# Optimization experiments

Measured on AMD Instinct MI355X. Metric: run time of the kernel, lower is better.

## Reference

```python
import jax, jax.numpy as jnp
import numpy as np

EPS = 1e-8
LAM = 100.0
SINKHORN_ITER = 50


def _sinkhorn(pred, target, cost, lam, n_iter):
    # pred: (B, na), target: (B, nb), cost: (na, nb)
    na = pred.shape[1]
    nb = target.shape[1]
    cost = cost[:na, :nb]
    K = jnp.exp(-cost / lam)          # (na, nb)
    KM = cost * K                      # (na, nb)
    B = pred.shape[0]
    log_a = jnp.log(pred + EPS)
    log_b = jnp.log(target + EPS)
    log_u0 = jnp.full((B, na), -np.log(na), dtype=pred.dtype)
    log_v0 = jnp.full((B, nb), -np.log(nb), dtype=pred.dtype)

    def cond(state):
        i, _, _, done = state
        return (i < n_iter) & jnp.logical_not(done)

    def body(state):
        i, log_u, log_v, done = state
        log_u_max = jnp.max(log_u, axis=1, keepdims=True)
        # NOTE: original code adds EPS inside the exp here (kept for fidelity)
        u_stab = jnp.exp(log_u - log_u_max + EPS)
        # torch.mm(K.t(), u_stab.t()).t() == u_stab @ K
        log_v_new = log_b - jnp.log(u_stab @ K) - log_u_max
        log_v_max = jnp.max(log_v_new, axis=1, keepdims=True)
        v_stab = jnp.exp(log_v_new - log_v_max)
        log_u_new = log_a - jnp.log(v_stab @ K.T + EPS) - log_v_max
        # early-exit convergence check (relative Frobenius norm)
        done_new = (jnp.linalg.norm(log_u - log_u_new) /
                    jnp.linalg.norm(log_u_new)) < EPS
        return (i + 1, log_u_new, log_v_new, done_new)

    _, log_u, log_v, _ = jax.lax.while_loop(
        cond, body, (jnp.int32(0), log_u0, log_v0, jnp.array(False)))

    log_v_max = jnp.max(log_v, axis=1, keepdims=True)
    v_stab = jnp.exp(log_v - log_v_max)
    logcostpart1 = jnp.log(v_stab @ KM.T + EPS) + log_v_max
    wnorm = jnp.exp(log_u + logcostpart1).mean(0).sum()
    grad_input = log_u * lam
    grad_input = grad_input - grad_input.mean(axis=1, keepdims=True)
    grad_input = grad_input - grad_input.mean(axis=1, keepdims=True)
    grad_input = grad_input / B
    return wnorm.reshape(1), grad_input


def setup_inputs() -> dict:
    key = jax.random.key(0)
    k1, k2, k3 = jax.random.split(key, 3)
    B, na, nb = 65536, 128, 128
    pred = jax.random.uniform(k1, (B, na), dtype=jnp.float32)
    target = jax.random.uniform(k2, (B, nb), dtype=jnp.float32)
    cost = jax.random.uniform(k3, (na, nb), dtype=jnp.float32)
    return {"pred": pred, "target": target, "cost": cost}


def reference(pred, target, cost):
    return _sinkhorn(pred, target, cost, LAM, SINKHORN_ITER)
```

## Files before the change

kernel.cpp:

```cpp
#include <hip/hip_runtime.h>
#include <hip/hip_bf16.h>


typedef __attribute__((ext_vector_type(4))) float f32x4;
typedef __attribute__((ext_vector_type(4))) short s16x4;
typedef __attribute__((ext_vector_type(8))) short s16x8;

constexpr int   BLOCK = 512;
constexpr float EPSF  = 1e-8f;
constexpr float LOG2E = 1.44269504088896340736f;
constexpr float LN2   = 0.69314718055994530942f;
constexpr float GRADS = LN2 * 100.0f / 65536.0f;


#define SGB_PAIR() do {                                      \
    __builtin_amdgcn_sched_group_barrier(0x100, 2, 0);       \
    __builtin_amdgcn_sched_group_barrier(0x008, 1, 0);       \
  } while (0)

__device__ __forceinline__ unsigned short f2bf(float x) {
  unsigned u = __builtin_bit_cast(unsigned, x);
  u += 0x7fffu + ((u >> 16) & 1u);
  return (unsigned short)(u >> 16);
}
__device__ __forceinline__ float bf2f(short h) {
  return __builtin_bit_cast(float, (unsigned)(unsigned short)h << 16);
}
__device__ __forceinline__ short f2bf_hot(float x) {
  return __builtin_bit_cast(short, __float2bfloat16(x));
}

__device__ __forceinline__ int swzw(int r, int c) {
  return (r << 7) + ((((c >> 2) ^ ((r & 7) << 2)) << 2) | (c & 3));
}

__device__ __forceinline__ s16x8 afrag(const short* M, int row, int kb, int h) {
  const int base = (row << 7) + ((((kb >> 2) + h) ^ ((row & 7) << 2)) << 2);
  const s16x4 lo = *reinterpret_cast<const s16x4*>(M + base);
  const s16x4 hi = *reinterpret_cast<const s16x4*>(M + (base ^ 16));
  s16x8 r;
  r[0] = lo[0]; r[1] = lo[1]; r[2] = lo[2]; r[3] = lo[3];
  r[4] = hi[0]; r[5] = hi[1]; r[6] = hi[2]; r[7] = hi[3];
  return r;
}

__device__ __forceinline__ s16x8 packb(const f32x4 a, const f32x4 b) {
  s16x8 r;
  r[0] = f2bf_hot(a[0]); r[1] = f2bf_hot(a[1]);
  r[2] = f2bf_hot(a[2]); r[3] = f2bf_hot(a[3]);
  r[4] = f2bf_hot(b[0]); r[5] = f2bf_hot(b[1]);
  r[6] = f2bf_hot(b[2]); r[7] = f2bf_hot(b[3]);
  return r;
}

__global__ __launch_bounds__(256)
void sink_pre(const float* __restrict__ cost, unsigned short* __restrict__ wh,
              float* __restrict__ Sf)
{
  const float c1 = LOG2E * 0.01f;
  const int tid = threadIdx.x;
  if (blockIdx.x < 32) {
    for (int idx = blockIdx.x * 256 + tid; idx < 16384; idx += 8192) {
      const int r = idx >> 7, c = idx & 127;
      const float cst = cost[idx];
      const float k   = __builtin_amdgcn_exp2f(-cst * c1);
      const unsigned short eb = f2bf(k - 1.0f);
      wh[swzw(r, c)]          = eb;
      wh[16384 + swzw(c, r)]  = eb;
      wh[32768 + swzw(r, c)]  = f2bf(cst * k);
    }
  } else {
    __shared__ float ps[256];
    const int i = tid & 127, jh = tid >> 7;
    float s = 0.f;
#pragma unroll 8
    for (int j = jh * 64; j < jh * 64 + 64; ++j)
      s += __builtin_amdgcn_exp2f(-cost[(j << 7) + i] * c1);
    ps[tid] = s;
    __syncthreads();
    if (tid < 128) Sf[tid] = ps[tid] + ps[tid + 128];
  }
}

__global__ __launch_bounds__(BLOCK, 4)
void sink_mfma(const float* __restrict__ pred,
               const float* __restrict__ tgt,
               const unsigned short* __restrict__ wh,
               const float* __restrict__ Sf,
               float* __restrict__ out,
               float* __restrict__ wsf)
{
  __shared__ __align__(16) short EA[128 * 128];
  __shared__ __align__(16) short EB[128 * 128];
  __shared__ float wred[8];

  const int tid  = threadIdx.x;
  const int lane = tid & 63;
  const int wv   = tid >> 6;
  const int cl   = lane & 15;
  const int h    = lane >> 4;

  const int row0 = (blockIdx.x << 7) + (wv << 4);
  const int rr   = (row0 + cl) << 7;

  float4 p4[8], t4[8], s4[8];
#pragma unroll
  for (int mt = 0; mt < 8; ++mt) {
    p4[mt] = *reinterpret_cast<const float4*>(&pred[rr + (mt << 4) + (h << 2)]);
    t4[mt] = *reinterpret_cast<const float4*>(&tgt [rr + (mt << 4) + (h << 2)]);
    s4[mt] = *reinterpret_cast<const float4*>(&Sf[(mt << 4) + (h << 2)]);
  }

  {
    const uint4* gB = reinterpret_cast<const uint4*>(wh);
    const uint4* gA = reinterpret_cast<const uint4*>(wh + 16384);
    uint4* lB = reinterpret_cast<uint4*>(EB);
    uint4* lA = reinterpret_cast<uint4*>(EA);
#pragma unroll
    for (int k = 0; k < 4; ++k) {
      lB[tid + k * BLOCK] = gB[tid + k * BLOCK];
      lA[tid + k * BLOCK] = gA[tid + k * BLOCK];
    }
  }

  s16x8 ab[4], bb[4], vf[4], uf[4];
  f32x4 X[8];
  float sum_v = 0.f;
#pragma unroll
  for (int mt = 0; mt < 8; ++mt) {
    f32x4 qa, qb, v;
    qa[0] = p4[mt].x + EPSF; qa[1] = p4[mt].y + EPSF;
    qa[2] = p4[mt].z + EPSF; qa[3] = p4[mt].w + EPSF;
    qb[0] = t4[mt].x + EPSF; qb[1] = t4[mt].y + EPSF;
    qb[2] = t4[mt].z + EPSF; qb[3] = t4[mt].w + EPSF;
    v[0] = qb[0] * __builtin_amdgcn_rcpf(s4[mt].x);
    v[1] = qb[1] * __builtin_amdgcn_rcpf(s4[mt].y);
    v[2] = qb[2] * __builtin_amdgcn_rcpf(s4[mt].z);
    v[3] = qb[3] * __builtin_amdgcn_rcpf(s4[mt].w);
    sum_v += v[0] + v[1] + v[2] + v[3];
    X[mt] = v;
#pragma unroll
    for (int q = 0; q < 4; ++q) {
      ab[mt >> 1][(mt & 1) * 4 + q] = f2bf_hot(qa[q]);
      bb[mt >> 1][(mt & 1) * 4 + q] = f2bf_hot(qb[q]);
    }
  }
#pragma unroll
  for (int s = 0; s < 4; ++s) vf[s] = packb(X[2 * s], X[2 * s + 1]);
  sum_v += __shfl_xor(sum_v, 16);
  sum_v += __shfl_xor(sum_v, 32);
  __syncthreads();

#pragma unroll
  for (int mt = 0; mt < 8; ++mt) X[mt] = f32x4{0, 0, 0, 0};
#pragma unroll
  for (int s = 0; s < 4; ++s)
#pragma unroll
    for (int mt = 0; mt < 8; ++mt) {
      X[mt] = __builtin_amdgcn_mfma_f32_16x16x32_bf16(
          afrag(EB, cl + (mt << 4), s << 5, h), vf[s], X[mt], 0, 0, 0);
      SGB_PAIR();
    }
  float sum_u = 0.f;
#pragma unroll
  for (int mt = 0; mt < 8; ++mt)
#pragma unroll
    for (int q = 0; q < 4; ++q) {
      const float a = bf2f(ab[mt >> 1][(mt & 1) * 4 + q]);
      const float r = a * __builtin_amdgcn_rcpf(sum_v + X[mt][q] + EPSF);
      X[mt][q] = r;
      sum_u += r;
    }
#pragma unroll
  for (int s = 0; s < 4; ++s) uf[s] = packb(X[2 * s], X[2 * s + 1]);
  sum_u += __shfl_xor(sum_u, 16);
  sum_u += __shfl_xor(sum_u, 32);

#pragma unroll
  for (int mt = 0; mt < 8; ++mt) X[mt] = f32x4{0, 0, 0, 0};
#pragma unroll
  for (int s = 0; s < 4; ++s)
#pragma unroll
    for (int mt = 0; mt < 8; ++mt) {
      X[mt] = __builtin_amdgcn_mfma_f32_16x16x32_bf16(
          afrag(EA, cl + (mt << 4), s << 5, h), uf[s], X[mt], 0, 0, 0);
      SGB_PAIR();
    }
  sum_v = 0.f;
#pragma unroll
  for (int mt = 0; mt < 8; ++mt)
#pragma unroll
    for (int q = 0; q < 4; ++q) {
      const float b = bf2f(bb[mt >> 1][(mt & 1) * 4 + q]);
      const float v = b * __builtin_amdgcn_rcpf(sum_u + X[mt][q]);
      X[mt][q] = v;
      sum_v += v;
    }
#pragma unroll
  for (int s = 0; s < 4; ++s) vf[s] = packb(X[2 * s], X[2 * s + 1]);
  sum_v += __shfl_xor(sum_v, 16);
  sum_v += __shfl_xor(sum_v, 32);

#pragma unroll
  for (int mt = 0; mt < 8; ++mt) X[mt] = f32x4{0, 0, 0, 0};
#pragma unroll
  for (int s = 0; s < 4; ++s)
#pragma unroll
    for (int mt = 0; mt < 8; ++mt) {
      X[mt] = __builtin_amdgcn_mfma_f32_16x16x32_bf16(
          afrag(EB, cl + (mt << 4), s << 5, h), vf[s], X[mt], 0, 0, 0);
      SGB_PAIR();
    }
#pragma unroll
  for (int mt = 0; mt < 8; ++mt)
#pragma unroll
    for (int q = 0; q < 4; ++q) {
      const float a = bf2f(ab[mt >> 1][(mt & 1) * 4 + q]);
      X[mt][q] = a * __builtin_amdgcn_rcpf(sum_v + X[mt][q] + EPSF);
    }

  __syncthreads();
  {
    const uint4* gK = reinterpret_cast<const uint4*>(wh + 32768);
    uint4* lB = reinterpret_cast<uint4*>(EB);
#pragma unroll
    for (int k = 0; k < 4; ++k) lB[tid + k * BLOCK] = gK[tid + k * BLOCK];
  }
  __syncthreads();

  f32x4 T[8];
#pragma unroll
  for (int mt = 0; mt < 8; ++mt) T[mt] = f32x4{0, 0, 0, 0};
#pragma unroll
  for (int s = 0; s < 4; ++s)
#pragma unroll
    for (int mt = 0; mt < 8; ++mt) {
      T[mt] = __builtin_amdgcn_mfma_f32_16x16x32_bf16(
          afrag(EB, cl + (mt << 4), s << 5, h), vf[s], T[mt], 0, 0, 0);
      SGB_PAIR();
    }

  float wsum = 0.f;
#pragma unroll
  for (int mt = 0; mt < 8; ++mt)
#pragma unroll
    for (int q = 0; q < 4; ++q)
      wsum += X[mt][q] * (T[mt][q] + EPSF);
  wsum += __shfl_xor(wsum, 1);
  wsum += __shfl_xor(wsum, 2);
  wsum += __shfl_xor(wsum, 4);
  wsum += __shfl_xor(wsum, 8);
  wsum += __shfl_xor(wsum, 16);
  wsum += __shfl_xor(wsum, 32);
  if (lane == 0) wred[wv] = wsum;

  {
#pragma unroll
    for (int mt = 0; mt < 8; ++mt)
#pragma unroll
      for (int q = 0; q < 4; ++q)
        X[mt][q] = __builtin_amdgcn_logf(X[mt][q]);
    float sm = 0.f;
#pragma unroll
    for (int mt = 0; mt < 8; ++mt)
#pragma unroll
      for (int q = 0; q < 4; ++q) sm += X[mt][q];
    sm += __shfl_xor(sm, 16);
    sm += __shfl_xor(sm, 32);
    const float mean = sm * 0.0078125f;

    float* TAf = reinterpret_cast<float*>(EA);
    const int obase = 1 + (blockIdx.x << 14);
    const int lrow  = (wv & 3) << 4;
#pragma unroll
    for (int half = 0; half < 2; ++half) {
      __syncthreads();
      if ((wv >> 2) == half) {
#pragma unroll
        for (int mt = 0; mt < 8; ++mt)
#pragma unroll
          for (int q = 0; q < 4; ++q) {
            const int col = (mt << 4) + (h << 2) + q;
            TAf[((lrow + cl) << 7) + (col ^ ((cl & 7) << 2))] =
                (X[mt][q] - mean) * GRADS;
          }
      }
      __syncthreads();
#pragma unroll
      for (int k = 0; k < 16; ++k) {
        const int lin = k * BLOCK + tid;
        const int row = lin >> 7, col = lin & 127;
        out[obase + (half << 13) + lin] =
            TAf[(row << 7) + (col ^ ((row & 7) << 2))];
      }
    }
  }

  __syncthreads();
  if (tid == 0) {
    float s = 0.f;
#pragma unroll
    for (int w = 0; w < 8; ++w) s += wred[w];
    wsf[blockIdx.x] = s;
  }
}

__global__ void sink_reduce(const float* __restrict__ wsf, float* __restrict__ out)
{
  float s = 0.f;
  for (int i = threadIdx.x; i < 512; i += 256) s += wsf[i];
  s += __shfl_xor(s, 1);
  s += __shfl_xor(s, 2);
  s += __shfl_xor(s, 4);
  s += __shfl_xor(s, 8);
  s += __shfl_xor(s, 16);
  s += __shfl_xor(s, 32);
  __shared__ float sm[4];
  if ((threadIdx.x & 63) == 0) sm[threadIdx.x >> 6] = s;
  __syncthreads();
  if (threadIdx.x == 0) out[0] = (sm[0] + sm[1] + sm[2] + sm[3]) * (1.0f / 65536.0f);
}

extern "C" void kernel_launch(void* const* d_in, const int* in_sizes, int n_in,
                              void* d_out, int out_size, void* d_ws, size_t ws_size,
                              hipStream_t stream)
{
  const float* pred = (const float*)d_in[0];
  const float* tgt  = (const float*)d_in[1];
  const float* cost = (const float*)d_in[2];
  float* out = (float*)d_out;
  unsigned short* wh = (unsigned short*)d_ws;
  float* Sf  = ((float*)d_ws) + 24576;
  float* wsf = ((float*)d_ws) + 24704;

  sink_pre<<<33, 256, 0, stream>>>(cost, wh, Sf);
  sink_mfma<<<512, BLOCK, 0, stream>>>(pred, tgt, wh, Sf, out, wsf);
  sink_reduce<<<1, 256, 0, stream>>>(wsf, out);
}
```

Measured before the change: 44.77 us.

## Process two row tiles per block with all tables resident in LDS

Each block now handles 256 rows in two sequential tiles instead of 128 rows. All three bf16 tables (E, E^T, K*M) are loaded into LDS once, so the block no longer reloads the cost table mid-kernel behind extra barriers. The next tile's pred and target are prefetched during the current tile. The final E and KM matmuls are fused into one interleaved MFMA loop, and the output transpose goes through a per-wave LDS buffer without block-wide barriers. In exchange the grid halves to 256 blocks, shared memory per block grows, and the launch-bounds occupancy hint drops to 2, which may cut latency hiding.

```diff
diff --git a/kernel.cpp b/kernel.cpp
--- a/kernel.cpp
+++ b/kernel.cpp
@@ -16,6 +16,10 @@
 #define SGB_PAIR() do {                                      \
     __builtin_amdgcn_sched_group_barrier(0x100, 2, 0);       \
     __builtin_amdgcn_sched_group_barrier(0x008, 1, 0);       \
+  } while (0)
+#define SGB_QUAD() do {                                      \
+    __builtin_amdgcn_sched_group_barrier(0x100, 4, 0);       \
+    __builtin_amdgcn_sched_group_barrier(0x008, 2, 0);       \
   } while (0)
 
 __device__ __forceinline__ unsigned short f2bf(float x) {
@@ -82,7 +86,7 @@
   }
 }
 
-__global__ __launch_bounds__(BLOCK, 4)
+__global__ __launch_bounds__(BLOCK, 2)
 void sink_mfma(const float* __restrict__ pred,
                const float* __restrict__ tgt,
                const unsigned short* __restrict__ wh,
@@ -90,9 +94,12 @@
                float* __restrict__ out,
                float* __restrict__ wsf)
 {
-  __shared__ __align__(16) short EA[128 * 128];
-  __shared__ __align__(16) short EB[128 * 128];
-  __shared__ float wred[8];
+  __shared__ __align__(16) short TBL[3 * 16384];
+  __shared__ __align__(16) float TR[8 * 1024];
+
+  const short* Es  = TBL;
+  const short* ETs = TBL + 16384;
+  const short* KMs = TBL + 32768;
 
   const int tid  = threadIdx.x;
   const int lane = tid & 63;
@@ -100,207 +107,196 @@
   const int cl   = lane & 15;
   const int h    = lane >> 4;
 
-  const int row0 = (blockIdx.x << 7) + (wv << 4);
-  const int rr   = (row0 + cl) << 7;
-
-  float4 p4[8], t4[8], s4[8];
+  const int rr0 = (((blockIdx.x << 8) + (wv << 4) + cl) << 7) + (h << 2);
+  float4 p4[8], t4[8], rs[8];
 #pragma unroll
   for (int mt = 0; mt < 8; ++mt) {
-    p4[mt] = *reinterpret_cast<const float4*>(&pred[rr + (mt << 4) + (h << 2)]);
-    t4[mt] = *reinterpret_cast<const float4*>(&tgt [rr + (mt << 4) + (h << 2)]);
-    s4[mt] = *reinterpret_cast<const float4*>(&Sf[(mt << 4) + (h << 2)]);
+    p4[mt] = *reinterpret_cast<const float4*>(&pred[rr0 + (mt << 4)]);
+    t4[mt] = *reinterpret_cast<const float4*>(&tgt [rr0 + (mt << 4)]);
+    const float4 s = *reinterpret_cast<const float4*>(&Sf[(mt << 4) + (h << 2)]);
+    rs[mt].x = __builtin_amdgcn_rcpf(s.x);
+    rs[mt].y = __builtin_amdgcn_rcpf(s.y);
+    rs[mt].z = __builtin_amdgcn_rcpf(s.z);
+    rs[mt].w = __builtin_amdgcn_rcpf(s.w);
   }
 
   {
-    const uint4* gB = reinterpret_cast<const uint4*>(wh);
-    const uint4* gA = reinterpret_cast<const uint4*>(wh + 16384);
-    uint4* lB = reinterpret_cast<uint4*>(EB);
-    uint4* lA = reinterpret_cast<uint4*>(EA);
-#pragma unroll
-    for (int k = 0; k < 4; ++k) {
-      lB[tid + k * BLOCK] = gB[tid + k * BLOCK];
-      lA[tid + k * BLOCK] = gA[tid + k * BLOCK];
-    }
-  }
-
-  s16x8 ab[4], bb[4], vf[4], uf[4];
-  f32x4 X[8];
-  float sum_v = 0.f;
-#pragma unroll
-  for (int mt = 0; mt < 8; ++mt) {
-    f32x4 qa, qb, v;
-    qa[0] = p4[mt].x + EPSF; qa[1] = p4[mt].y + EPSF;
-    qa[2] = p4[mt].z + EPSF; qa[3] = p4[mt].w + EPSF;
-    qb[0] = t4[mt].x + EPSF; qb[1] = t4[mt].y + EPSF;
-    qb[2] = t4[mt].z + EPSF; qb[3] = t4[mt].w + EPSF;
-    v[0] = qb[0] * __builtin_amdgcn_rcpf(s4[mt].x);
-    v[1] = qb[1] * __builtin_amdgcn_rcpf(s4[mt].y);
-    v[2] = qb[2] * __builtin_amdgcn_rcpf(s4[mt].z);
-    v[3] = qb[3] * __builtin_amdgcn_rcpf(s4[mt].w);
-    sum_v += v[0] + v[1] + v[2] + v[3];
-    X[mt] = v;
-#pragma unroll
-    for (int q = 0; q < 4; ++q) {
-      ab[mt >> 1][(mt & 1) * 4 + q] = f2bf_hot(qa[q]);
-      bb[mt >> 1][(mt & 1) * 4 + q] = f2bf_hot(qb[q]);
-    }
-  }
-#pragma unroll
-  for (int s = 0; s < 4; ++s) vf[s] = packb(X[2 * s], X[2 * s + 1]);
-  sum_v += __shfl_xor(sum_v, 16);
-  sum_v += __shfl_xor(sum_v, 32);
+    const uint4* g = reinterpret_cast<const uint4*>(wh);
+    uint4* l = reinterpret_cast<uint4*>(TBL);
+#pragma unroll
+    for (int k = 0; k < 12; ++k) l[tid + k * BLOCK] = g[tid + k * BLOCK];
+  }
   __syncthreads();
 
-#pragma unroll
-  for (int mt = 0; mt < 8; ++mt) X[mt] = f32x4{0, 0, 0, 0};
-#pragma unroll
-  for (int s = 0; s < 4; ++s)
+  float wacc = 0.f;
+  float* TRw = TR + (wv << 10);
+
+#pragma unroll
+  for (int tile = 0; tile < 2; ++tile) {
+    s16x8 ab[4], bb[4], vf[4], uf[4];
+    f32x4 X[8], T[8];
+    float sum_v = 0.f;
 #pragma unroll
     for (int mt = 0; mt < 8; ++mt) {
-      X[mt] = __builtin_amdgcn_mfma_f32_16x16x32_bf16(
-          afrag(EB, cl + (mt << 4), s << 5, h), vf[s], X[mt], 0, 0, 0);
-      SGB_PAIR();
-    }
-  float sum_u = 0.f;
-#pragma unroll
-  for (int mt = 0; mt < 8; ++mt)
-#pragma unroll
-    for (int q = 0; q < 4; ++q) {
-      const float a = bf2f(ab[mt >> 1][(mt & 1) * 4 + q]);
-      const float r = a * __builtin_amdgcn_rcpf(sum_v + X[mt][q] + EPSF);
-      X[mt][q] = r;
-      sum_u += r;
-    }
-#pragma unroll
-  for (int s = 0; s < 4; ++s) uf[s] = packb(X[2 * s], X[2 * s + 1]);
-  sum_u += __shfl_xor(sum_u, 16);
-  sum_u += __shfl_xor(sum_u, 32);
-
-#pragma unroll
-  for (int mt = 0; mt < 8; ++mt) X[mt] = f32x4{0, 0, 0, 0};
-#pragma unroll
-  for (int s = 0; s < 4; ++s)
+      f32x4 qa, qb, v;
+      qa[0] = p4[mt].x + EPSF; qa[1] = p4[mt].y + EPSF;
+      qa[2] = p4[mt].z + EPSF; qa[3] = p4[mt].w + EPSF;
+      qb[0] = t4[mt].x + EPSF; qb[1] = t4[mt].y + EPSF;
+      qb[2] = t4[mt].z + EPSF; qb[3] = t4[mt].w + EPSF;
+      v[0] = qb[0] * rs[mt].x; v[1] = qb[1] * rs[mt].y;
+      v[2] = qb[2] * rs[mt].z; v[3] = qb[3] * rs[mt].w;
+      sum_v += v[0] + v[1] + v[2] + v[3];
+      X[mt] = v;
+#pragma unroll
+      for (int q = 0; q < 4; ++q) {
+        ab[mt >> 1][(mt & 1) * 4 + q] = f2bf_hot(qa[q]);
+        bb[mt >> 1][(mt & 1) * 4 + q] = f2bf_hot(qb[q]);
+      }
+    }
+#pragma unroll
+    for (int s = 0; s < 4; ++s) vf[s] = packb(X[2 * s], X[2 * s + 1]);
+    sum_v += __shfl_xor(sum_v, 16);
+    sum_v += __shfl_xor(sum_v, 32);
+
+    if (tile == 0) {
+      const int rr1 = rr0 + (128 << 7);
+#pragma unroll
+      for (int mt = 0; mt < 8; ++mt) {
+        p4[mt] = *reinterpret_cast<const float4*>(&pred[rr1 + (mt << 4)]);
+        t4[mt] = *reinterpret_cast<const float4*>(&tgt [rr1 + (mt << 4)]);
+      }
+    }
+
+#pragma unroll
+    for (int mt = 0; mt < 8; ++mt) X[mt] = f32x4{0, 0, 0, 0};
+#pragma unroll
+    for (int s = 0; s < 4; ++s)
+#pragma unroll
+      for (int mt = 0; mt < 8; ++mt) {
+        X[mt] = __builtin_amdgcn_mfma_f32_16x16x32_bf16(
+            afrag(Es, cl + (mt << 4), s << 5, h), vf[s], X[mt], 0, 0, 0);
+        SGB_PAIR();
+      }
+    float sum_u = 0.f;
+#pragma unroll
+    for (int mt = 0; mt < 8; ++mt)
+#pragma unroll
+      for (int q = 0; q < 4; ++q) {
+        const float a = bf2f(ab[mt >> 1][(mt & 1) * 4 + q]);
+        const float r = a * __builtin_amdgcn_rcpf(sum_v + X[mt][q] + EPSF);
+        X[mt][q] = r;
+        sum_u += r;
+      }
+#pragma unroll
+    for (int s = 0; s < 4; ++s) uf[s] = packb(X[2 * s], X[2 * s + 1]);
+    sum_u += __shfl_xor(sum_u, 16);
+    sum_u += __shfl_xor(sum_u, 32);
+
+#pragma unroll
+    for (int mt = 0; mt < 8; ++mt) X[mt] = f32x4{0, 0, 0, 0};
+#pragma unroll
+    for (int s = 0; s < 4; ++s)
+#pragma unroll
+      for (int mt = 0; mt < 8; ++mt) {
+        X[mt] = __builtin_amdgcn_mfma_f32_16x16x32_bf16(
+            afrag(ETs, cl + (mt << 4), s << 5, h), uf[s], X[mt], 0, 0, 0);
+        SGB_PAIR();
+      }
+    sum_v = 0.f;
+#pragma unroll
+    for (int mt = 0; mt < 8; ++mt)
+#pragma unroll
+      for (int q = 0; q < 4; ++q) {
+        const float b = bf2f(bb[mt >> 1][(mt & 1) * 4 + q]);
+        const float v = b * __builtin_amdgcn_rcpf(sum_u + X[mt][q]);
+        X[mt][q] = v;
+        sum_v += v;
+      }
+#pragma unroll
+    for (int s = 0; s < 4; ++s) vf[s] = packb(X[2 * s], X[2 * s + 1]);
+    sum_v += __shfl_xor(sum_v, 16);
+    sum_v += __shfl_xor(sum_v, 32);
+
 #pragma unroll
     for (int mt = 0; mt < 8; ++mt) {
-      X[mt] = __builtin_amdgcn_mfma_f32_16x16x32_bf16(
-          afrag(EA, cl + (mt << 4), s << 5, h), uf[s], X[mt], 0, 0, 0);
-      SGB_PAIR();
-    }
-  sum_v = 0.f;
-#pragma unroll
-  for (int mt = 0; mt < 8; ++mt)
-#pragma unroll
-    for (int q = 0; q < 4; ++q) {
-      const float b = bf2f(bb[mt >> 1][(mt & 1) * 4 + q]);
-      const float v = b * __builtin_amdgcn_rcpf(sum_u + X[mt][q]);
-      X[mt][q] = v;
-      sum_v += v;
-    }
-#pragma unroll
-  for (int s = 0; s < 4; ++s) vf[s] = packb(X[2 * s], X[2 * s + 1]);
-  sum_v += __shfl_xor(sum_v, 16);
-  sum_v += __shfl_xor(sum_v, 32);
-
-#pragma unroll
-  for (int mt = 0; mt < 8; ++mt) X[mt] = f32x4{0, 0, 0, 0};
-#pragma unroll
-  for (int s = 0; s < 4; ++s)
-#pragma unroll
-    for (int mt = 0; mt < 8; ++mt) {
-      X[mt] = __builtin_amdgcn_mfma_f32_16x16x32_bf16(
-          afrag(EB, cl + (mt << 4), s << 5, h), vf[s], X[mt], 0, 0, 0);
-      SGB_PAIR();
-    }
-#pragma unroll
-  for (int mt = 0; mt < 8; ++mt)
-#pragma unroll
-    for (int q = 0; q < 4; ++q) {
-      const float a = bf2f(ab[mt >> 1][(mt & 1) * 4 + q]);
-      X[mt][q] = a * __builtin_amdgcn_rcpf(sum_v + X[mt][q] + EPSF);
-    }
-
+      X[mt] = f32x4{0, 0, 0, 0};
+      T[mt] = f32x4{0, 0, 0, 0};
+    }
+#pragma unroll
+    for (int s = 0; s < 4; ++s)
+#pragma unroll
+      for (int mt = 0; mt < 8; ++mt) {
+        X[mt] = __builtin_amdgcn_mfma_f32_16x16x32_bf16(
+            afrag(Es, cl + (mt << 4), s << 5, h), vf[s], X[mt], 0, 0, 0);
+        T[mt] = __builtin_amdgcn_mfma_f32_16x16x32_bf16(
+            afrag(KMs, cl + (mt << 4), s << 5, h), vf[s], T[mt], 0, 0, 0);
+        SGB_QUAD();
+      }
+#pragma unroll
+    for (int mt = 0; mt < 8; ++mt)
+#pragma unroll
+      for (int q = 0; q < 4; ++q) {
+        const float a = bf2f(ab[mt >> 1][(mt & 1) * 4 + q]);
+        X[mt][q] = a * __builtin_amdgcn_rcpf(sum_v + X[mt][q] + EPSF);
+      }
+
+#pragma unroll
+    for (int mt = 0; mt < 8; ++mt)
+#pragma unroll
+      for (int q = 0; q < 4; ++q)
+        wacc += X[mt][q] * (T[mt][q] + EPSF);
+
+    {
+#pragma unroll
+      for (int mt = 0; mt < 8; ++mt)
+#pragma unroll
+        for (int q = 0; q < 4; ++q)
+          X[mt][q] = __builtin_amdgcn_logf(X[mt][q]);
+      float sm = 0.f;
+#pragma unroll
+      for (int mt = 0; mt < 8; ++mt)
+#pragma unroll
+        for (int q = 0; q < 4; ++q) sm += X[mt][q];
+      sm += __shfl_xor(sm, 16);
+      sm += __shfl_xor(sm, 32);
+      const float mean = sm * 0.0078125f;
+
+      const int owave = 1 + ((((blockIdx.x << 1) + tile) << 7) + (wv << 4)) * 128;
+      const int rloc = cl & 7;
+#pragma unroll
+      for (int p = 0; p < 2; ++p) {
+        if ((cl >> 3) == p) {
+#pragma unroll
+          for (int mt = 0; mt < 8; ++mt)
+#pragma unroll
+            for (int q = 0; q < 4; ++q) {
+              const int col = (mt << 4) + (h << 2) + q;
+              TRw[(rloc << 7) + (col ^ (rloc << 2))] = (X[mt][q] - mean) * GRADS;
+            }
+        }
+#pragma unroll
+        for (int k = 0; k < 16; ++k) {
+          const int lin = k * 64 + lane;
+          const int r = lin >> 7, c = lin & 127;
+          out[owave + (p << 10) + lin] = TRw[(r << 7) + (c ^ (r << 2))];
+        }
+      }
+    }
+  }
+
+  wacc += __shfl_xor(wacc, 1);
+  wacc += __shfl_xor(wacc, 2);
+  wacc += __shfl_xor(wacc, 4);
+  wacc += __shfl_xor(wacc, 8);
+  wacc += __shfl_xor(wacc, 16);
+  wacc += __shfl_xor(wacc, 32);
   __syncthreads();
-  {
-    const uint4* gK = reinterpret_cast<const uint4*>(wh + 32768);
-    uint4* lB = reinterpret_cast<uint4*>(EB);
-#pragma unroll
-    for (int k = 0; k < 4; ++k) lB[tid + k * BLOCK] = gK[tid + k * BLOCK];
-  }
-  __syncthreads();
-
-  f32x4 T[8];
-#pragma unroll
-  for (int mt = 0; mt < 8; ++mt) T[mt] = f32x4{0, 0, 0, 0};
-#pragma unroll
-  for (int s = 0; s < 4; ++s)
-#pragma unroll
-    for (int mt = 0; mt < 8; ++mt) {
-      T[mt] = __builtin_amdgcn_mfma_f32_16x16x32_bf16(
-          afrag(EB, cl + (mt << 4), s << 5, h), vf[s], T[mt], 0, 0, 0);
-      SGB_PAIR();
-    }
-
-  float wsum = 0.f;
-#pragma unroll
-  for (int mt = 0; mt < 8; ++mt)
-#pragma unroll
-    for (int q = 0; q < 4; ++q)
-      wsum += X[mt][q] * (T[mt][q] + EPSF);
-  wsum += __shfl_xor(wsum, 1);
-  wsum += __shfl_xor(wsum, 2);
-  wsum += __shfl_xor(wsum, 4);
-  wsum += __shfl_xor(wsum, 8);
-  wsum += __shfl_xor(wsum, 16);
-  wsum += __shfl_xor(wsum, 32);
-  if (lane == 0) wred[wv] = wsum;
-
-  {
-#pragma unroll
-    for (int mt = 0; mt < 8; ++mt)
-#pragma unroll
-      for (int q = 0; q < 4; ++q)
-        X[mt][q] = __builtin_amdgcn_logf(X[mt][q]);
-    float sm = 0.f;
-#pragma unroll
-    for (int mt = 0; mt < 8; ++mt)
-#pragma unroll
-      for (int q = 0; q < 4; ++q) sm += X[mt][q];
-    sm += __shfl_xor(sm, 16);
-    sm += __shfl_xor(sm, 32);
-    const float mean = sm * 0.0078125f;
-
-    float* TAf = reinterpret_cast<float*>(EA);
-    const int obase = 1 + (blockIdx.x << 14);
-    const int lrow  = (wv & 3) << 4;
-#pragma unroll
-    for (int half = 0; half < 2; ++half) {
-      __syncthreads();
-      if ((wv >> 2) == half) {
-#pragma unroll
-        for (int mt = 0; mt < 8; ++mt)
-#pragma unroll
-          for (int q = 0; q < 4; ++q) {
-            const int col = (mt << 4) + (h << 2) + q;
-            TAf[((lrow + cl) << 7) + (col ^ ((cl & 7) << 2))] =
-                (X[mt][q] - mean) * GRADS;
-          }
-      }
-      __syncthreads();
-#pragma unroll
-      for (int k = 0; k < 16; ++k) {
-        const int lin = k * BLOCK + tid;
-        const int row = lin >> 7, col = lin & 127;
-        out[obase + (half << 13) + lin] =
-            TAf[(row << 7) + (col ^ ((row & 7) << 2))];
-      }
-    }
-  }
-
+  if (lane == 0) TR[wv] = wacc;
   __syncthreads();
   if (tid == 0) {
     float s = 0.f;
 #pragma unroll
-    for (int w = 0; w < 8; ++w) s += wred[w];
+    for (int w = 0; w < 8; ++w) s += TR[w];
     wsf[blockIdx.x] = s;
   }
 }
@@ -308,7 +304,7 @@
 __global__ void sink_reduce(const float* __restrict__ wsf, float* __restrict__ out)
 {
   float s = 0.f;
-  for (int i = threadIdx.x; i < 512; i += 256) s += wsf[i];
+  for (int i = threadIdx.x; i < 256; i += 256) s += wsf[i];
   s += __shfl_xor(s, 1);
   s += __shfl_xor(s, 2);
   s += __shfl_xor(s, 4);
@@ -334,6 +330,6 @@
   float* wsf = ((float*)d_ws) + 24704;
 
   sink_pre<<<33, 256, 0, stream>>>(cost, wh, Sf);
-  sink_mfma<<<512, BLOCK, 0, stream>>>(pred, tgt, wh, Sf, out, wsf);
+  sink_mfma<<<256, BLOCK, 0, stream>>>(pred, tgt, wh, Sf, out, wsf);
   sink_reduce<<<1, 256, 0, stream>>>(wsf, out);
 }
```

After: 59.02 us. 31.8% more time.

## Fuse final reduction into main kernel via last-block atomic; prefetch KM weights

Applied to the files above, without the earlier changes.

Removes the separate sink_reduce launch by having each block publish its partial sum with a release store and bump an atomic counter, so the last block finishes the reduction. The KM weight matrix is now read from global memory into registers at kernel start and written into the freed EA buffer before the final Sinkhorn matvec, which removes one global-load stall and one barrier. MFMA/LDS-read scheduling barriers are regrouped from pairs into groups of eight. The cost is extra register pressure from holding KM in registers, plus a counter reset in the pre-kernel.

```diff
diff --git a/kernel.cpp b/kernel.cpp
--- a/kernel.cpp
+++ b/kernel.cpp
@@ -13,9 +13,9 @@
 constexpr float GRADS = LN2 * 100.0f / 65536.0f;
 
 
-#define SGB_PAIR() do {                                      \
-    __builtin_amdgcn_sched_group_barrier(0x100, 2, 0);       \
-    __builtin_amdgcn_sched_group_barrier(0x008, 1, 0);       \
+#define SGB_G8() do {                                        \
+    __builtin_amdgcn_sched_group_barrier(0x100, 8, 0);       \
+    __builtin_amdgcn_sched_group_barrier(0x008, 4, 0);       \
   } while (0)
 
 __device__ __forceinline__ unsigned short f2bf(float x) {
@@ -55,7 +55,7 @@
 
 __global__ __launch_bounds__(256)
 void sink_pre(const float* __restrict__ cost, unsigned short* __restrict__ wh,
-              float* __restrict__ Sf)
+              float* __restrict__ Sf, unsigned* __restrict__ cnt)
 {
   const float c1 = LOG2E * 0.01f;
   const int tid = threadIdx.x;
@@ -70,6 +70,7 @@
       wh[32768 + swzw(r, c)]  = f2bf(cst * k);
     }
   } else {
+    if (tid == 0) *cnt = 0u;
     __shared__ float ps[256];
     const int i = tid & 127, jh = tid >> 7;
     float s = 0.f;
@@ -88,11 +89,13 @@
                const unsigned short* __restrict__ wh,
                const float* __restrict__ Sf,
                float* __restrict__ out,
-               float* __restrict__ wsf)
+               float* __restrict__ wsf,
+               unsigned* __restrict__ cnt)
 {
   __shared__ __align__(16) short EA[128 * 128];
   __shared__ __align__(16) short EB[128 * 128];
   __shared__ float wred[8];
+  __shared__ unsigned lastflag;
 
   const int tid  = threadIdx.x;
   const int lane = tid & 63;
@@ -104,11 +107,17 @@
   const int rr   = (row0 + cl) << 7;
 
   float4 p4[8], t4[8], s4[8];
+  uint4 kmr[4];
 #pragma unroll
   for (int mt = 0; mt < 8; ++mt) {
     p4[mt] = *reinterpret_cast<const float4*>(&pred[rr + (mt << 4) + (h << 2)]);
     t4[mt] = *reinterpret_cast<const float4*>(&tgt [rr + (mt << 4) + (h << 2)]);
     s4[mt] = *reinterpret_cast<const float4*>(&Sf[(mt << 4) + (h << 2)]);
+  }
+  {
+    const uint4* gK = reinterpret_cast<const uint4*>(wh + 32768);
+#pragma unroll
+    for (int k = 0; k < 4; ++k) kmr[k] = gK[tid + k * BLOCK];
   }
 
   {
@@ -159,7 +168,7 @@
     for (int mt = 0; mt < 8; ++mt) {
       X[mt] = __builtin_amdgcn_mfma_f32_16x16x32_bf16(
           afrag(EB, cl + (mt << 4), s << 5, h), vf[s], X[mt], 0, 0, 0);
-      SGB_PAIR();
+      if ((mt & 3) == 3) SGB_G8();
     }
   float sum_u = 0.f;
 #pragma unroll
@@ -184,7 +193,7 @@
     for (int mt = 0; mt < 8; ++mt) {
       X[mt] = __builtin_amdgcn_mfma_f32_16x16x32_bf16(
           afrag(EA, cl + (mt << 4), s << 5, h), uf[s], X[mt], 0, 0, 0);
-      SGB_PAIR();
+      if ((mt & 3) == 3) SGB_G8();
     }
   sum_v = 0.f;
 #pragma unroll
@@ -201,6 +210,13 @@
   sum_v += __shfl_xor(sum_v, 16);
   sum_v += __shfl_xor(sum_v, 32);
 
+  __syncthreads();
+  {
+    uint4* lA = reinterpret_cast<uint4*>(EA);
+#pragma unroll
+    for (int k = 0; k < 4; ++k) lA[tid + k * BLOCK] = kmr[k];
+  }
+
 #pragma unroll
   for (int mt = 0; mt < 8; ++mt) X[mt] = f32x4{0, 0, 0, 0};
 #pragma unroll
@@ -209,7 +225,7 @@
     for (int mt = 0; mt < 8; ++mt) {
       X[mt] = __builtin_amdgcn_mfma_f32_16x16x32_bf16(
           afrag(EB, cl + (mt << 4), s << 5, h), vf[s], X[mt], 0, 0, 0);
-      SGB_PAIR();
+      if ((mt & 3) == 3) SGB_G8();
     }
 #pragma unroll
   for (int mt = 0; mt < 8; ++mt)
@@ -218,14 +234,6 @@
       const float a = bf2f(ab[mt >> 1][(mt & 1) * 4 + q]);
       X[mt][q] = a * __builtin_amdgcn_rcpf(sum_v + X[mt][q] + EPSF);
     }
-
-  __syncthreads();
-  {
-    const uint4* gK = reinterpret_cast<const uint4*>(wh + 32768);
-    uint4* lB = reinterpret_cast<uint4*>(EB);
-#pragma unroll
-    for (int k = 0; k < 4; ++k) lB[tid + k * BLOCK] = gK[tid + k * BLOCK];
-  }
   __syncthreads();
 
   f32x4 T[8];
@@ -236,8 +244,8 @@
 #pragma unroll
     for (int mt = 0; mt < 8; ++mt) {
       T[mt] = __builtin_amdgcn_mfma_f32_16x16x32_bf16(
-          afrag(EB, cl + (mt << 4), s << 5, h), vf[s], T[mt], 0, 0, 0);
-      SGB_PAIR();
+          afrag(EA, cl + (mt << 4), s << 5, h), vf[s], T[mt], 0, 0, 0);
+      if ((mt & 3) == 3) SGB_G8();
     }
 
   float wsum = 0.f;
@@ -301,24 +309,26 @@
     float s = 0.f;
 #pragma unroll
     for (int w = 0; w < 8; ++w) s += wred[w];
-    wsf[blockIdx.x] = s;
-  }
-}
-
-__global__ void sink_reduce(const float* __restrict__ wsf, float* __restrict__ out)
-{
-  float s = 0.f;
-  for (int i = threadIdx.x; i < 512; i += 256) s += wsf[i];
-  s += __shfl_xor(s, 1);
-  s += __shfl_xor(s, 2);
-  s += __shfl_xor(s, 4);
-  s += __shfl_xor(s, 8);
-  s += __shfl_xor(s, 16);
-  s += __shfl_xor(s, 32);
-  __shared__ float sm[4];
-  if ((threadIdx.x & 63) == 0) sm[threadIdx.x >> 6] = s;
-  __syncthreads();
-  if (threadIdx.x == 0) out[0] = (sm[0] + sm[1] + sm[2] + sm[3]) * (1.0f / 65536.0f);
+    __hip_atomic_store(&wsf[blockIdx.x], s, __ATOMIC_RELEASE,
+                       __HIP_MEMORY_SCOPE_AGENT);
+    const unsigned prev = __hip_atomic_fetch_add(cnt, 1u, __ATOMIC_ACQ_REL,
+                                                 __HIP_MEMORY_SCOPE_AGENT);
+    lastflag = (prev == 511u) ? 1u : 0u;
+  }
+  __syncthreads();
+  if (lastflag != 0u && wv == 0) {
+    float s = 0.f;
+    for (int i = lane; i < 512; i += 64)
+      s += __hip_atomic_load(&wsf[i], __ATOMIC_ACQUIRE,
+                             __HIP_MEMORY_SCOPE_AGENT);
+    s += __shfl_xor(s, 1);
+    s += __shfl_xor(s, 2);
+    s += __shfl_xor(s, 4);
+    s += __shfl_xor(s, 8);
+    s += __shfl_xor(s, 16);
+    s += __shfl_xor(s, 32);
+    if (lane == 0) out[0] = s * (1.0f / 65536.0f);
+  }
 }
 
 extern "C" void kernel_launch(void* const* d_in, const int* in_sizes, int n_in,
@@ -332,8 +342,8 @@
   unsigned short* wh = (unsigned short*)d_ws;
   float* Sf  = ((float*)d_ws) + 24576;
   float* wsf = ((float*)d_ws) + 24704;
-
-  sink_pre<<<33, 256, 0, stream>>>(cost, wh, Sf);
-  sink_mfma<<<512, BLOCK, 0, stream>>>(pred, tgt, wh, Sf, out, wsf);
-  sink_reduce<<<1, 256, 0, stream>>>(wsf, out);
-}
+  unsigned* cnt = (unsigned*)(((float*)d_ws) + 25216);
+
+  sink_pre<<<33, 256, 0, stream>>>(cost, wh, Sf, cnt);
+  sink_mfma<<<512, BLOCK, 0, stream>>>(pred, tgt, wh, Sf, out, wsf, cnt);
+}
```

Result: slower. 101.8 us (+127.5%).

## Process two 16-row tiles per wave to reuse LDS A-fragments across MFMAs

Applied to the files above, without the earlier changes.

Halves the block to 256 threads, with each wave now handling 32 rows as two 16-row N-tiles. Each A-fragment read from LDS feeds two MFMAs, halving LDS traffic per MFMA, and the schedule barrier is adjusted to pair 2 MFMAs with 2 LDS reads. Reciprocals of the column sums are hoisted and shared. The cost is doubled accumulator and fragment register use with launch bounds dropped to 2 blocks per CU, which lowers occupancy and the latency hiding it provides.

```diff
diff --git a/kernel.cpp b/kernel.cpp
--- a/kernel.cpp
+++ b/kernel.cpp
@@ -6,16 +6,16 @@
 typedef __attribute__((ext_vector_type(4))) short s16x4;
 typedef __attribute__((ext_vector_type(8))) short s16x8;
 
-constexpr int   BLOCK = 512;
+constexpr int   BLOCK = 256;
 constexpr float EPSF  = 1e-8f;
 constexpr float LOG2E = 1.44269504088896340736f;
 constexpr float LN2   = 0.69314718055994530942f;
 constexpr float GRADS = LN2 * 100.0f / 65536.0f;
 
 
-#define SGB_PAIR() do {                                      \
+#define SGB_22() do {                                        \
     __builtin_amdgcn_sched_group_barrier(0x100, 2, 0);       \
-    __builtin_amdgcn_sched_group_barrier(0x008, 1, 0);       \
+    __builtin_amdgcn_sched_group_barrier(0x008, 2, 0);       \
   } while (0)
 
 __device__ __forceinline__ unsigned short f2bf(float x) {
@@ -82,7 +82,7 @@
   }
 }
 
-__global__ __launch_bounds__(BLOCK, 4)
+__global__ __launch_bounds__(BLOCK, 2)
 void sink_mfma(const float* __restrict__ pred,
                const float* __restrict__ tgt,
                const unsigned short* __restrict__ wh,
@@ -92,7 +92,7 @@
 {
   __shared__ __align__(16) short EA[128 * 128];
   __shared__ __align__(16) short EB[128 * 128];
-  __shared__ float wred[8];
+  __shared__ float wred[4];
 
   const int tid  = threadIdx.x;
   const int lane = tid & 63;
@@ -100,15 +100,24 @@
   const int cl   = lane & 15;
   const int h    = lane >> 4;
 
-  const int row0 = (blockIdx.x << 7) + (wv << 4);
-  const int rr   = (row0 + cl) << 7;
-
-  float4 p4[8], t4[8], s4[8];
+  const int row0 = (blockIdx.x << 7) + (wv << 5);
+
+  float4 rs[8], p4[8], t4[8];
 #pragma unroll
   for (int mt = 0; mt < 8; ++mt) {
-    p4[mt] = *reinterpret_cast<const float4*>(&pred[rr + (mt << 4) + (h << 2)]);
-    t4[mt] = *reinterpret_cast<const float4*>(&tgt [rr + (mt << 4) + (h << 2)]);
-    s4[mt] = *reinterpret_cast<const float4*>(&Sf[(mt << 4) + (h << 2)]);
+    const float4 s = *reinterpret_cast<const float4*>(&Sf[(mt << 4) + (h << 2)]);
+    rs[mt].x = __builtin_amdgcn_rcpf(s.x);
+    rs[mt].y = __builtin_amdgcn_rcpf(s.y);
+    rs[mt].z = __builtin_amdgcn_rcpf(s.z);
+    rs[mt].w = __builtin_amdgcn_rcpf(s.w);
+  }
+  {
+    const int rr = ((row0 + cl) << 7) + (h << 2);
+#pragma unroll
+    for (int mt = 0; mt < 8; ++mt) {
+      p4[mt] = *reinterpret_cast<const float4*>(&pred[rr + (mt << 4)]);
+      t4[mt] = *reinterpret_cast<const float4*>(&tgt [rr + (mt << 4)]);
+    }
   }
 
   {
@@ -117,177 +126,212 @@
     uint4* lB = reinterpret_cast<uint4*>(EB);
     uint4* lA = reinterpret_cast<uint4*>(EA);
 #pragma unroll
-    for (int k = 0; k < 4; ++k) {
+    for (int k = 0; k < 8; ++k) {
       lB[tid + k * BLOCK] = gB[tid + k * BLOCK];
       lA[tid + k * BLOCK] = gA[tid + k * BLOCK];
     }
   }
 
-  s16x8 ab[4], bb[4], vf[4], uf[4];
-  f32x4 X[8];
-  float sum_v = 0.f;
-#pragma unroll
-  for (int mt = 0; mt < 8; ++mt) {
-    f32x4 qa, qb, v;
-    qa[0] = p4[mt].x + EPSF; qa[1] = p4[mt].y + EPSF;
-    qa[2] = p4[mt].z + EPSF; qa[3] = p4[mt].w + EPSF;
-    qb[0] = t4[mt].x + EPSF; qb[1] = t4[mt].y + EPSF;
-    qb[2] = t4[mt].z + EPSF; qb[3] = t4[mt].w + EPSF;
-    v[0] = qb[0] * __builtin_amdgcn_rcpf(s4[mt].x);
-    v[1] = qb[1] * __builtin_amdgcn_rcpf(s4[mt].y);
-    v[2] = qb[2] * __builtin_amdgcn_rcpf(s4[mt].z);
-    v[3] = qb[3] * __builtin_amdgcn_rcpf(s4[mt].w);
-    sum_v += v[0] + v[1] + v[2] + v[3];
-    X[mt] = v;
-#pragma unroll
-    for (int q = 0; q < 4; ++q) {
-      ab[mt >> 1][(mt & 1) * 4 + q] = f2bf_hot(qa[q]);
-      bb[mt >> 1][(mt & 1) * 4 + q] = f2bf_hot(qb[q]);
-    }
-  }
-#pragma unroll
-  for (int s = 0; s < 4; ++s) vf[s] = packb(X[2 * s], X[2 * s + 1]);
-  sum_v += __shfl_xor(sum_v, 16);
-  sum_v += __shfl_xor(sum_v, 32);
-  __syncthreads();
-
-#pragma unroll
-  for (int mt = 0; mt < 8; ++mt) X[mt] = f32x4{0, 0, 0, 0};
+  s16x8 ab[2][4], bb[2][4], vf[2][4], uf[2][4];
+  f32x4 X[2][8];
+  float sum_v[2], sum_u[2];
+#pragma unroll
+  for (int nt = 0; nt < 2; ++nt) {
+    if (nt == 1) {
+      const int rr = ((row0 + 16 + cl) << 7) + (h << 2);
+#pragma unroll
+      for (int mt = 0; mt < 8; ++mt) {
+        p4[mt] = *reinterpret_cast<const float4*>(&pred[rr + (mt << 4)]);
+        t4[mt] = *reinterpret_cast<const float4*>(&tgt [rr + (mt << 4)]);
+      }
+    }
+    float sv = 0.f;
+#pragma unroll
+    for (int mt = 0; mt < 8; ++mt) {
+      f32x4 qa, qb, v;
+      qa[0] = p4[mt].x + EPSF; qa[1] = p4[mt].y + EPSF;
+      qa[2] = p4[mt].z + EPSF; qa[3] = p4[mt].w + EPSF;
+      qb[0] = t4[mt].x + EPSF; qb[1] = t4[mt].y + EPSF;
+      qb[2] = t4[mt].z + EPSF; qb[3] = t4[mt].w + EPSF;
+      v[0] = qb[0] * rs[mt].x; v[1] = qb[1] * rs[mt].y;
+      v[2] = qb[2] * rs[mt].z; v[3] = qb[3] * rs[mt].w;
+      sv += v[0] + v[1] + v[2] + v[3];
+      X[nt][mt] = v;
+#pragma unroll
+      for (int q = 0; q < 4; ++q) {
+        ab[nt][mt >> 1][(mt & 1) * 4 + q] = f2bf_hot(qa[q]);
+        bb[nt][mt >> 1][(mt & 1) * 4 + q] = f2bf_hot(qb[q]);
+      }
+    }
+#pragma unroll
+    for (int s = 0; s < 4; ++s) vf[nt][s] = packb(X[nt][2 * s], X[nt][2 * s + 1]);
+    sv += __shfl_xor(sv, 16);
+    sv += __shfl_xor(sv, 32);
+    sum_v[nt] = sv;
+  }
+  __syncthreads();
+
+#pragma unroll
+  for (int mt = 0; mt < 8; ++mt) { X[0][mt] = f32x4{0,0,0,0}; X[1][mt] = f32x4{0,0,0,0}; }
 #pragma unroll
   for (int s = 0; s < 4; ++s)
 #pragma unroll
     for (int mt = 0; mt < 8; ++mt) {
-      X[mt] = __builtin_amdgcn_mfma_f32_16x16x32_bf16(
-          afrag(EB, cl + (mt << 4), s << 5, h), vf[s], X[mt], 0, 0, 0);
-      SGB_PAIR();
-    }
-  float sum_u = 0.f;
-#pragma unroll
-  for (int mt = 0; mt < 8; ++mt)
-#pragma unroll
-    for (int q = 0; q < 4; ++q) {
-      const float a = bf2f(ab[mt >> 1][(mt & 1) * 4 + q]);
-      const float r = a * __builtin_amdgcn_rcpf(sum_v + X[mt][q] + EPSF);
-      X[mt][q] = r;
-      sum_u += r;
-    }
-#pragma unroll
-  for (int s = 0; s < 4; ++s) uf[s] = packb(X[2 * s], X[2 * s + 1]);
-  sum_u += __shfl_xor(sum_u, 16);
-  sum_u += __shfl_xor(sum_u, 32);
-
-#pragma unroll
-  for (int mt = 0; mt < 8; ++mt) X[mt] = f32x4{0, 0, 0, 0};
+      const s16x8 a = afrag(EB, cl + (mt << 4), s << 5, h);
+      X[0][mt] = __builtin_amdgcn_mfma_f32_16x16x32_bf16(a, vf[0][s], X[0][mt], 0, 0, 0);
+      X[1][mt] = __builtin_amdgcn_mfma_f32_16x16x32_bf16(a, vf[1][s], X[1][mt], 0, 0, 0);
+      SGB_22();
+    }
+#pragma unroll
+  for (int nt = 0; nt < 2; ++nt) {
+    float su = 0.f;
+#pragma unroll
+    for (int mt = 0; mt < 8; ++mt)
+#pragma unroll
+      for (int q = 0; q < 4; ++q) {
+        const float a = bf2f(ab[nt][mt >> 1][(mt & 1) * 4 + q]);
+        const float r = a * __builtin_amdgcn_rcpf(sum_v[nt] + X[nt][mt][q] + EPSF);
+        X[nt][mt][q] = r;
+        su += r;
+      }
+#pragma unroll
+    for (int s = 0; s < 4; ++s) uf[nt][s] = packb(X[nt][2 * s], X[nt][2 * s + 1]);
+    su += __shfl_xor(su, 16);
+    su += __shfl_xor(su, 32);
+    sum_u[nt] = su;
+  }
+
+#pragma unroll
+  for (int mt = 0; mt < 8; ++mt) { X[0][mt] = f32x4{0,0,0,0}; X[1][mt] = f32x4{0,0,0,0}; }
 #pragma unroll
   for (int s = 0; s < 4; ++s)
 #pragma unroll
     for (int mt = 0; mt < 8; ++mt) {
-      X[mt] = __builtin_amdgcn_mfma_f32_16x16x32_bf16(
-          afrag(EA, cl + (mt << 4), s << 5, h), uf[s], X[mt], 0, 0, 0);
-      SGB_PAIR();
-    }
-  sum_v = 0.f;
-#pragma unroll
-  for (int mt = 0; mt < 8; ++mt)
-#pragma unroll
-    for (int q = 0; q < 4; ++q) {
-      const float b = bf2f(bb[mt >> 1][(mt & 1) * 4 + q]);
-      const float v = b * __builtin_amdgcn_rcpf(sum_u + X[mt][q]);
-      X[mt][q] = v;
-      sum_v += v;
-    }
-#pragma unroll
-  for (int s = 0; s < 4; ++s) vf[s] = packb(X[2 * s], X[2 * s + 1]);
-  sum_v += __shfl_xor(sum_v, 16);
-  sum_v += __shfl_xor(sum_v, 32);
-
-#pragma unroll
-  for (int mt = 0; mt < 8; ++mt) X[mt] = f32x4{0, 0, 0, 0};
+      const s16x8 a = afrag(EA, cl + (mt << 4), s << 5, h);
+      X[0][mt] = __builtin_amdgcn_mfma_f32_16x16x32_bf16(a, uf[0][s], X[0][mt], 0, 0, 0);
+      X[1][mt] = __builtin_amdgcn_mfma_f32_16x16x32_bf16(a, uf[1][s], X[1][mt], 0, 0, 0);
+      SGB_22();
+    }
+#pragma unroll
+  for (int nt = 0; nt < 2; ++nt) {
+    float sv = 0.f;
+#pragma unroll
+    for (int mt = 0; mt < 8; ++mt)
+#pragma unroll
+      for (int q = 0; q < 4; ++q) {
+        const float b = bf2f(bb[nt][mt >> 1][(mt & 1) * 4 + q]);
+        const float v = b * __builtin_amdgcn_rcpf(sum_u[nt] + X[nt][mt][q]);
+        X[nt][mt][q] = v;
+        sv += v;
+      }
+#pragma unroll
+    for (int s = 0; s < 4; ++s) vf[nt][s] = packb(X[nt][2 * s], X[nt][2 * s + 1]);
+    sv += __shfl_xor(sv, 16);
+    sv += __shfl_xor(sv, 32);
+    sum_v[nt] = sv;
+  }
+
+#pragma unroll
+  for (int mt = 0; mt < 8; ++mt) { X[0][mt] = f32x4{0,0,0,0}; X[1][mt] = f32x4{0,0,0,0}; }
 #pragma unroll
   for (int s = 0; s < 4; ++s)
 #pragma unroll
     for (int mt = 0; mt < 8; ++mt) {
-      X[mt] = __builtin_amdgcn_mfma_f32_16x16x32_bf16(
-          afrag(EB, cl + (mt << 4), s << 5, h), vf[s], X[mt], 0, 0, 0);
-      SGB_PAIR();
-    }
-#pragma unroll
-  for (int mt = 0; mt < 8; ++mt)
-#pragma unroll
-    for (int q = 0; q < 4; ++q) {
-      const float a = bf2f(ab[mt >> 1][(mt & 1) * 4 + q]);
-      X[mt][q] = a * __builtin_amdgcn_rcpf(sum_v + X[mt][q] + EPSF);
-    }
+      const s16x8 a = afrag(EB, cl + (mt << 4), s << 5, h);
+      X[0][mt] = __builtin_amdgcn_mfma_f32_16x16x32_bf16(a, vf[0][s], X[0][mt], 0, 0, 0);
+      X[1][mt] = __builtin_amdgcn_mfma_f32_16x16x32_bf16(a, vf[1][s], X[1][mt], 0, 0, 0);
+      SGB_22();
+    }
+#pragma unroll
+  for (int nt = 0; nt < 2; ++nt)
+#pragma unroll
+    for (int mt = 0; mt < 8; ++mt)
+#pragma unroll
+      for (int q = 0; q < 4; ++q) {
+        const float a = bf2f(ab[nt][mt >> 1][(mt & 1) * 4 + q]);
+        X[nt][mt][q] = a * __builtin_amdgcn_rcpf(sum_v[nt] + X[nt][mt][q] + EPSF);
+      }
 
   __syncthreads();
   {
     const uint4* gK = reinterpret_cast<const uint4*>(wh + 32768);
     uint4* lB = reinterpret_cast<uint4*>(EB);
 #pragma unroll
-    for (int k = 0; k < 4; ++k) lB[tid + k * BLOCK] = gK[tid + k * BLOCK];
-  }
-  __syncthreads();
-
-  f32x4 T[8];
-#pragma unroll
-  for (int mt = 0; mt < 8; ++mt) T[mt] = f32x4{0, 0, 0, 0};
-#pragma unroll
-  for (int s = 0; s < 4; ++s)
-#pragma unroll
-    for (int mt = 0; mt < 8; ++mt) {
-      T[mt] = __builtin_amdgcn_mfma_f32_16x16x32_bf16(
-          afrag(EB, cl + (mt << 4), s << 5, h), vf[s], T[mt], 0, 0, 0);
-      SGB_PAIR();
-    }
-
-  float wsum = 0.f;
-#pragma unroll
-  for (int mt = 0; mt < 8; ++mt)
-#pragma unroll
-    for (int q = 0; q < 4; ++q)
-      wsum += X[mt][q] * (T[mt][q] + EPSF);
-  wsum += __shfl_xor(wsum, 1);
-  wsum += __shfl_xor(wsum, 2);
-  wsum += __shfl_xor(wsum, 4);
-  wsum += __shfl_xor(wsum, 8);
-  wsum += __shfl_xor(wsum, 16);
-  wsum += __shfl_xor(wsum, 32);
-  if (lane == 0) wred[wv] = wsum;
-
-  {
-#pragma unroll
-    for (int mt = 0; mt < 8; ++mt)
-#pragma unroll
-      for (int q = 0; q < 4; ++q)
-        X[mt][q] = __builtin_amdgcn_logf(X[mt][q]);
-    float sm = 0.f;
-#pragma unroll
-    for (int mt = 0; mt < 8; ++mt)
-#pragma unroll
-      for (int q = 0; q < 4; ++q) sm += X[mt][q];
-    sm += __shfl_xor(sm, 16);
-    sm += __shfl_xor(sm, 32);
-    const float mean = sm * 0.0078125f;
+    for (int k = 0; k < 8; ++k) lB[tid + k * BLOCK] = gK[tid + k * BLOCK];
+  }
+  __syncthreads();
+
+  float wacc = 0.f;
+  {
+    f32x4 T[2][8];
+#pragma unroll
+    for (int mt = 0; mt < 8; ++mt) { T[0][mt] = f32x4{0,0,0,0}; T[1][mt] = f32x4{0,0,0,0}; }
+#pragma unroll
+    for (int s = 0; s < 4; ++s)
+#pragma unroll
+      for (int mt = 0; mt < 8; ++mt) {
+        const s16x8 a = afrag(EB, cl + (mt << 4), s << 5, h);
+        T[0][mt] = __builtin_amdgcn_mfma_f32_16x16x32_bf16(a, vf[0][s], T[0][mt], 0, 0, 0);
+        T[1][mt] = __builtin_amdgcn_mfma_f32_16x16x32_bf16(a, vf[1][s], T[1][mt], 0, 0, 0);
+        SGB_22();
+      }
+#pragma unroll
+    for (int nt = 0; nt < 2; ++nt)
+#pragma unroll
+      for (int mt = 0; mt < 8; ++mt)
+#pragma unroll
+        for (int q = 0; q < 4; ++q)
+          wacc += X[nt][mt][q] * (T[nt][mt][q] + EPSF);
+  }
+  wacc += __shfl_xor(wacc, 1);
+  wacc += __shfl_xor(wacc, 2);
+  wacc += __shfl_xor(wacc, 4);
+  wacc += __shfl_xor(wacc, 8);
+  wacc += __shfl_xor(wacc, 16);
+  wacc += __shfl_xor(wacc, 32);
+  if (lane == 0) wred[wv] = wacc;
+
+  {
+    float mean[2];
+#pragma unroll
+    for (int nt = 0; nt < 2; ++nt) {
+#pragma unroll
+      for (int mt = 0; mt < 8; ++mt)
+#pragma unroll
+        for (int q = 0; q < 4; ++q)
+          X[nt][mt][q] = __builtin_amdgcn_logf(X[nt][mt][q]);
+      float sm = 0.f;
+#pragma unroll
+      for (int mt = 0; mt < 8; ++mt)
+#pragma unroll
+        for (int q = 0; q < 4; ++q) sm += X[nt][mt][q];
+      sm += __shfl_xor(sm, 16);
+      sm += __shfl_xor(sm, 32);
+      mean[nt] = sm * 0.0078125f;
+    }
 
     float* TAf = reinterpret_cast<float*>(EA);
     const int obase = 1 + (blockIdx.x << 14);
-    const int lrow  = (wv & 3) << 4;
 #pragma unroll
     for (int half = 0; half < 2; ++half) {
       __syncthreads();
-      if ((wv >> 2) == half) {
-#pragma unroll
-        for (int mt = 0; mt < 8; ++mt)
-#pragma unroll
-          for (int q = 0; q < 4; ++q) {
-            const int col = (mt << 4) + (h << 2) + q;
-            TAf[((lrow + cl) << 7) + (col ^ ((cl & 7) << 2))] =
-                (X[mt][q] - mean) * GRADS;
-          }
+      if ((wv >> 1) == half) {
+        const int lrow0 = (wv & 1) << 5;
+#pragma unroll
+        for (int nt = 0; nt < 2; ++nt)
+#pragma unroll
+          for (int mt = 0; mt < 8; ++mt)
+#pragma unroll
+            for (int q = 0; q < 4; ++q) {
+              const int lrow = lrow0 + (nt << 4) + cl;
+              const int col  = (mt << 4) + (h << 2) + q;
+              TAf[(lrow << 7) + (col ^ ((lrow & 7) << 2))] =
+                  (X[nt][mt][q] - mean[nt]) * GRADS;
+            }
       }
       __syncthreads();
 #pragma unroll
-      for (int k = 0; k < 16; ++k) {
+      for (int k = 0; k < 32; ++k) {
         const int lin = k * BLOCK + tid;
         const int row = lin >> 7, col = lin & 127;
         out[obase + (half << 13) + lin] =
@@ -297,12 +341,8 @@
   }
 
   __syncthreads();
-  if (tid == 0) {
-    float s = 0.f;
-#pragma unroll
-    for (int w = 0; w < 8; ++w) s += wred[w];
-    wsf[blockIdx.x] = s;
-  }
+  if (tid == 0)
+    wsf[blockIdx.x] = wred[0] + wred[1] + wred[2] + wred[3];
 }
 
 __global__ void sink_reduce(const float* __restrict__ wsf, float* __restrict__ out)
```

New measurement: 46.91 us. 1.05x slower.
